# Kernel optimization log

Hardware: AMD Instinct MI355X
Metric: run time of the kernel (lower is better)

## Reference

```python
import jax, jax.numpy as jnp
import numpy as np

G = 8  # order of C8 rotation group

def expand_circulant(w):
    # w: [out_fields, in_fields, G] free params of a C8 regular->regular 1x1 conv.
    # Full weight: W[of*G+go, if*G+gi] = w[of, if, (go-gi) mod G]
    g = jnp.arange(G)
    idx = (g[:, None] - g[None, :]) % G            # [go, gi]
    Wf = w[:, :, idx]                              # [of, if, go, gi]
    Wf = jnp.transpose(Wf, (0, 2, 1, 3))           # [of, go, if, gi]
    return Wf.reshape(w.shape[0] * G, w.shape[1] * G)

def eq_proj(x2, w, b):
    # x2: [B, in_fields*G]; equivariant 1x1 conv = GEMM with circulant-expanded weight
    Wf = expand_circulant(w)                       # [out_fields*G, in_fields*G]
    bf = jnp.repeat(b, G)                          # per-field bias, shared across group dim
    return x2 @ Wf.T + bf

def setup_inputs() -> dict:
    key = jax.random.key(0)
    ks = jax.random.split(key, 12)
    B, d_model, n_head, d_k, d_v = 8192, 128, 8, 64, 64
    C = d_model * G                                # 1024
    s_in = 0.02
    inp = {
        'q': jax.random.normal(ks[0], (B, C, 1, 1), jnp.float32),
        'k': jax.random.normal(ks[1], (B, C, 1, 1), jnp.float32),
        'v': jax.random.normal(ks[2], (B, C, 1, 1), jnp.float32),
        'w_q': jax.random.normal(ks[3], (n_head * d_k, d_model, G), jnp.float32) * s_in,
        'b_q': jnp.zeros((n_head * d_k,), jnp.float32),
        'w_k': jax.random.normal(ks[4], (n_head * d_k, d_model, G), jnp.float32) * s_in,
        'b_k': jnp.zeros((n_head * d_k,), jnp.float32),
        'w_v': jax.random.normal(ks[5], (n_head * d_v, d_model, G), jnp.float32) * s_in,
        'b_v': jnp.zeros((n_head * d_v,), jnp.float32),
        'w_fc': jax.random.normal(ks[6], (d_model, n_head * d_v, G), jnp.float32) * s_in,
        'b_fc': jnp.zeros((d_model,), jnp.float32),
    }
    return inp

def reference(q, k, v, w_q, b_q, w_k, b_k, w_v, b_v, w_fc, b_fc):
    B, C = q.shape[0], q.shape[1]
    n_head, d_k = 8, 64
    d_v = 64
    temp = jnp.asarray(d_k ** 0.5, q.dtype)
    residual = q                                   # [B, C, 1, 1]
    q2 = q.reshape(B, C)
    k2 = k.reshape(B, C)
    v2 = v.reshape(B, C)
    # equivariant 1x1 conv projections -> [B, n_head*d_k*G]
    qp = eq_proj(q2, w_q, b_q).reshape(B, G, n_head, d_k).transpose(0, 2, 1, 3)  # [B,H,G,dk]
    kp = eq_proj(k2, w_k, b_k).reshape(B, G, n_head, d_k).transpose(0, 2, 1, 3)
    vp = eq_proj(v2, w_v, b_v).reshape(B, G, n_head, d_v).transpose(0, 2, 1, 3)
    # scaled dot-product attention over the G=8 group/orientation positions
    attn = jax.nn.softmax(jnp.einsum('bhqd,bhkd->bhqk', qp / temp, kp), axis=-1)  # [B,H,G,G]
    out = jnp.einsum('bhqk,bhkd->bhqd', attn, vp)  # [B,H,G,dv]
    # transpose(1,2) then flatten, exactly as torch .view(sz_b, -1, 1, 1)
    out = out.transpose(0, 2, 1, 3).reshape(B, G * n_head * d_v)
    out = eq_proj(out, w_fc, b_fc)                 # [B, d_model*G]
    out = out.reshape(B, C, 1, 1) + residual
    return out, attn
```

## Files before the change

kernel.cpp:

```cpp
#include <hip/hip_runtime.h>
#include <hip/hip_bf16.h>

typedef unsigned short u16;
typedef unsigned int u32;
typedef __bf16 bf16x8_t __attribute__((ext_vector_type(8)));
typedef float f32x4_t __attribute__((ext_vector_type(4)));

#define BK 64

__device__ __forceinline__ float b2f(u16 v) {
  return __uint_as_float(((u32)v) << 16);
}
__device__ __forceinline__ u16 f2b(float f) {
  __hip_bfloat16 h = __float2bfloat16(f);
  return *reinterpret_cast<u16*>(&h);
}
__device__ __forceinline__ float blo(u32 u) { return __uint_as_float(u << 16); }
__device__ __forceinline__ float bhi(u32 u) { return __uint_as_float(u & 0xffff0000u); }

__device__ __forceinline__ void async_lds16(const u16* g, u16* l) {
  __builtin_amdgcn_global_load_lds(
      (__attribute__((address_space(1))) void*)g,
      (__attribute__((address_space(3))) void*)l, 16, 0, 0);
}

__device__ __forceinline__ void expand8(const float* __restrict__ w,
                                        u16* __restrict__ dst, int I,
                                        int kshift, int gid) {
  const int n = gid >> kshift;
  const int kc = (gid & ((1 << kshift) - 1)) * 8;
  const int K = 8 << kshift;
  const float* wp = w + (size_t)((n >> 3) * I + (kc >> 3)) * 8;
  float4 w0 = *(const float4*)wp;
  float4 w1 = *(const float4*)(wp + 4);
  float w8[8] = {w0.x, w0.y, w0.z, w0.w, w1.x, w1.y, w1.z, w1.w};
  u16 t[8];
  const int r = (n - kc) & 7;
#pragma unroll
  for (int j = 0; j < 8; ++j) t[j] = f2b(w8[(r - j) & 7]);
  *(uint4*)(dst + (size_t)n * K + kc) = *(const uint4*)t;
}

__device__ __forceinline__ void cvt8(const float* __restrict__ src,
                                     u16* __restrict__ dst, int gid) {
  const float* p = src + (size_t)gid * 8;
  float4 a = *(const float4*)p;
  float4 b = *(const float4*)(p + 4);
  u16 t[8] = {f2b(a.x), f2b(a.y), f2b(a.z), f2b(a.w),
              f2b(b.x), f2b(b.y), f2b(b.z), f2b(b.w)};
  *(uint4*)(dst + (size_t)gid * 8) = *(const uint4*)t;
}

__global__ __launch_bounds__(256) void expand_all(
    const float* __restrict__ w_q, const float* __restrict__ w_k,
    const float* __restrict__ w_v, const float* __restrict__ w_fc,
    const float* __restrict__ q, const float* __restrict__ k,
    const float* __restrict__ v, u16* __restrict__ Wq, u16* __restrict__ Wk,
    u16* __restrict__ Wv, u16* __restrict__ Wfc, u16* __restrict__ qb,
    u16* __restrict__ kb, u16* __restrict__ vb, int cblocks) {
  const int e = blockIdx.x;
  if (e < 8192) {
    const int plane = e >> 11;
    const int gid = (e & 2047) * 256 + threadIdx.x;
    if (plane == 0) expand8(w_q, Wq, 128, 7, gid);
    else if (plane == 1) expand8(w_k, Wk, 128, 7, gid);
    else if (plane == 2) expand8(w_v, Wv, 128, 7, gid);
    else expand8(w_fc, Wfc, 512, 9, gid);
  } else {
    const int ce = e - 8192;
    const int plane = ce / cblocks;
    const int gid = (ce - plane * cblocks) * 256 + threadIdx.x;
    if (plane == 0) cvt8(q, qb, gid);
    else if (plane == 1) cvt8(k, kb, gid);
    else cvt8(v, vb, gid);
  }
}

__global__ __launch_bounds__(512, 2) void gemm_qkv256(
    const u16* __restrict__ X0, const u16* __restrict__ X1,
    const u16* __restrict__ X2, const u16* __restrict__ W0,
    const u16* __restrict__ W1, const u16* __restrict__ W2,
    const float* __restrict__ b0, const float* __restrict__ b1,
    const float* __restrict__ b2, u16* __restrict__ Y0, u16* __restrict__ Y1,
    u16* __restrict__ Y2, int M, int N, int K) {
  __shared__ __align__(16) u16 lds[4 * 16384];
  const int z = blockIdx.y;
  const u16* X = (z == 0) ? X0 : (z == 1) ? X1 : X2;
  const u16* W = (z == 0) ? W0 : (z == 1) ? W1 : W2;
  const float* bias = (z == 0) ? b0 : (z == 1) ? b1 : b2;
  u16* Y = (z == 0) ? Y0 : (z == 1) ? Y1 : Y2;

  const int tid = threadIdx.x;
  const int bid = blockIdx.x;
  const int grid_m = M >> 8, grid_n = N >> 8;
  const int nb = grid_m * grid_n;
  int pid = (bid & 7) * (nb >> 3) + (bid >> 3);
  const int nig = 8 * grid_n;
  const int group_id = pid / nig;
  const int first_m = group_id * 8;
  const int gsz = min(8, grid_m - first_m);
  const int mt = first_m + (pid % gsz);
  const int ntile = (pid % nig) / gsz;
  const int m0 = mt << 8, n0 = ntile << 8;

  const int lane = tid & 63, wave = tid >> 6;
  const int wm = (wave >> 2) * 128;
  const int wn = (wave & 3) * 64;
  const int l16 = lane & 15, quad = lane >> 4;
  const int kbl = quad ^ ((l16 >> 1) & 3);

  const int srow = tid >> 2;
  const int skbg = (tid & 3) ^ ((tid >> 3) & 3);
  const u16* pA = X + (size_t)(m0 + srow) * K + skbg * 8;
  const u16* pB = W + (size_t)(n0 + srow) * K + skbg * 8;
  const size_t rskip = (size_t)128 * K;

  const int aoff = (wm + l16) * 32 + kbl * 8;
  const int boff = 8192 + (wn + l16) * 32 + kbl * 8;

  f32x4_t acc[8][4] = {};
  const int nt = K >> 5;

  auto stage = [&](int t) {
    u16* l = lds + (t & 3) * 16384;
    const u16* a = pA + t * 32;
    const u16* b = pB + t * 32;
    async_lds16(a, l + tid * 8);
    async_lds16(a + rskip, l + tid * 8 + 4096);
    async_lds16(b, l + 8192 + tid * 8);
    async_lds16(b + rskip, l + 8192 + tid * 8 + 4096);
  };

  bf16x8_t A0[4], A1[4], Bc[4], Bn[4];

  stage(0);
  __builtin_amdgcn_sched_barrier(0);
  stage(1);
  __builtin_amdgcn_sched_barrier(0);
  stage(2);
  asm volatile("s_waitcnt vmcnt(4)" ::: "memory");
  __builtin_amdgcn_s_barrier();
  __builtin_amdgcn_sched_barrier(0);

  {
    const u16* la = lds + aoff;
    const u16* lb = lds + boff;
#pragma unroll
    for (int mi = 0; mi < 4; ++mi) A0[mi] = *(const bf16x8_t*)(la + mi * 512);
#pragma unroll
    for (int ni = 0; ni < 4; ++ni) Bc[ni] = *(const bf16x8_t*)(lb + ni * 512);
  }

  auto body = [&](int t, bf16x8_t (&BCUR)[4], bf16x8_t (&BNXT)[4]) {
    if (t + 3 < nt) stage(t + 3);
    const u16* lc = lds + (t & 3) * 16384;
    const u16* ln = lds + ((t + 1) & 3) * 16384;
#pragma unroll
    for (int mi = 0; mi < 4; ++mi)
      A1[mi] = *(const bf16x8_t*)(lc + aoff + (mi + 4) * 512);
    if (t + 1 < nt) {
#pragma unroll
      for (int ni = 0; ni < 4; ++ni)
        BNXT[ni] = *(const bf16x8_t*)(ln + boff + ni * 512);
    }
    __builtin_amdgcn_s_setprio(1);
#pragma unroll
    for (int mi = 0; mi < 4; ++mi)
#pragma unroll
      for (int ni = 0; ni < 4; ++ni)
        acc[mi][ni] = __builtin_amdgcn_mfma_f32_16x16x32_bf16(
            A0[mi], BCUR[ni], acc[mi][ni], 0, 0, 0);
    __builtin_amdgcn_s_setprio(0);
    if (t + 1 < nt) {
#pragma unroll
      for (int mi = 0; mi < 4; ++mi)
        A0[mi] = *(const bf16x8_t*)(ln + aoff + mi * 512);
    }
    __builtin_amdgcn_s_setprio(1);
#pragma unroll
    for (int mi = 0; mi < 4; ++mi)
#pragma unroll
      for (int ni = 0; ni < 4; ++ni)
        acc[mi + 4][ni] = __builtin_amdgcn_mfma_f32_16x16x32_bf16(
            A1[mi], BCUR[ni], acc[mi + 4][ni], 0, 0, 0);
    __builtin_amdgcn_s_setprio(0);
    if (t + 1 < nt) {
      asm volatile("s_waitcnt lgkmcnt(0)" ::: "memory");
      __builtin_amdgcn_sched_barrier(0);
      if (t + 3 < nt) asm volatile("s_waitcnt vmcnt(4)" ::: "memory");
      else            asm volatile("s_waitcnt vmcnt(0)" ::: "memory");
      __builtin_amdgcn_s_barrier();
      __builtin_amdgcn_sched_barrier(0);
    }
  };

  for (int t = 0; t < nt; t += 2) {
    body(t, Bc, Bn);
    body(t + 1, Bn, Bc);
  }

#pragma unroll
  for (int ni = 0; ni < 4; ++ni) {
    const int col = n0 + wn + ni * 16 + l16;
    const float bv = bias[col >> 3];
#pragma unroll
    for (int mi = 0; mi < 8; ++mi) {
#pragma unroll
      for (int r = 0; r < 4; ++r) {
        const int rw = m0 + wm + mi * 16 + quad * 4 + r;
        Y[(size_t)rw * N + col] = f2b(acc[mi][ni][r] + bv);
      }
    }
  }
}

template <int TN, bool HAS_RES, bool OUT_F32>
__device__ __forceinline__ void gemm_core(
    const u16* __restrict__ Xb, const u16* __restrict__ W,
    const float* __restrict__ bias, const float* __restrict__ res,
    void* __restrict__ Yv, int M, int N, int K, int bid) {
  __shared__ __align__(16) u16 As[128 * BK];
  __shared__ __align__(16) u16 Bs[TN * BK];
  const int tid = threadIdx.x;

  const int grid_m = M >> 7, grid_n = N / TN;
  const int nb = grid_m * grid_n;
  int pid = (bid & 7) * (nb >> 3) + (bid >> 3);
  const int nig = 8 * grid_n;
  const int group_id = pid / nig;
  const int first_m = group_id * 8;
  const int gsz = min(8, grid_m - first_m);
  const int mt = first_m + (pid % gsz);
  const int nt = (pid % nig) / gsz;
  const int m0 = mt << 7, n0 = nt * TN;

  const int lane = tid & 63;
  const int wave = tid >> 6;
  const int wm = (wave >> 1) * 64;
  const int wn = (wave & 1) * (TN / 2);
  const int l16 = lane & 15;
  const int quad = lane >> 4;
  constexpr int NJ = TN >> 5;

  f32x4_t acc[4][NJ] = {};

  const int row0 = tid >> 3;
  const int kgl = ((tid & 7) ^ (row0 & 7)) * 8;

  for (int k0 = 0; k0 < K; k0 += BK) {
#pragma unroll
    for (int it = 0; it < TN / 32; ++it)
      async_lds16(W + (size_t)(n0 + row0 + it * 32) * K + (k0 + kgl),
                  &Bs[(tid + it * 256) * 8]);
#pragma unroll
    for (int it = 0; it < 4; ++it)
      async_lds16(Xb + (size_t)(m0 + row0 + it * 32) * K + (k0 + kgl),
                  &As[(tid + it * 256) * 8]);
    __syncthreads();
#pragma unroll
    for (int half = 0; half < 2; ++half) {
      bf16x8_t af[4], bfr[NJ];
#pragma unroll
      for (int i = 0; i < 4; ++i)
        af[i] = *(const bf16x8_t*)&As[(wm + i * 16 + l16) * BK +
                                      (((quad + half * 4) ^ (l16 & 7)) * 8)];
#pragma unroll
      for (int j = 0; j < NJ; ++j)
        bfr[j] = *(const bf16x8_t*)&Bs[(wn + j * 16 + l16) * BK +
                                       (((quad + half * 4) ^ (l16 & 7)) * 8)];
#pragma unroll
      for (int i = 0; i < 4; ++i)
#pragma unroll
        for (int j = 0; j < NJ; ++j)
          acc[i][j] =
              __builtin_amdgcn_mfma_f32_16x16x32_bf16(af[i], bfr[j], acc[i][j], 0, 0, 0);
    }
    __syncthreads();
  }

#pragma unroll
  for (int j = 0; j < NJ; ++j) {
    const int col = n0 + wn + j * 16 + l16;
    const float bv = bias[col >> 3];
#pragma unroll
    for (int i = 0; i < 4; ++i) {
#pragma unroll
      for (int r = 0; r < 4; ++r) {
        const int rw = m0 + wm + i * 16 + quad * 4 + r;
        float vv = acc[i][j][r] + bv;
        if (HAS_RES) vv += res[(size_t)rw * N + col];
        if (OUT_F32)
          ((float*)Yv)[(size_t)rw * N + col] = vv;
        else
          ((u16*)Yv)[(size_t)rw * N + col] = f2b(vv);
      }
    }
  }
}

__global__ __launch_bounds__(256) void gemm_fc(
    const u16* __restrict__ X, const u16* __restrict__ W,
    const float* __restrict__ bias, const float* __restrict__ res,
    float* __restrict__ Y, int M, int N, int K) {
  gemm_core<64, true, true>(X, W, bias, res, Y, M, N, K, blockIdx.x);
}

__global__ __launch_bounds__(256) void attn_kernel(
    const u16* __restrict__ qp, const u16* __restrict__ kp,
    const u16* __restrict__ vp, float* __restrict__ probs,
    u16* __restrict__ o, int iters) {
  __shared__ __align__(16) u16 Qs[4][8 * 72];
  __shared__ __align__(16) u16 Ks[4][8 * 72];
  __shared__ __align__(16) float Ps[4][64];
  const int tid = threadIdx.x;
  const int wave = tid >> 6;
  const int lane = tid & 63;
  const int r = lane >> 3, c = lane & 7;
  const int ls = r * 72 + c * 8;
  const int qg = r;
  const int kg = c;

  auto pairof = [&](int it) { return (it * gridDim.x + blockIdx.x) * 4 + wave; };
  auto gaddr = [&](int it) {
    const int pr = pairof(it);
    return (size_t)(pr >> 3) * 4096 + (size_t)r * 512 + (pr & 7) * 64 + c * 8;
  };

  uint4 qr = *(const uint4*)(qp + gaddr(0));
  uint4 kr = *(const uint4*)(kp + gaddr(0));

  for (int it = 0; it < iters; ++it) {
    *(uint4*)&Qs[wave][ls] = qr;
    *(uint4*)&Ks[wave][ls] = kr;
    const int pair = pairof(it);
    const int b = pair >> 3;
    const int h = pair & 7;
    float vcf[8];
#pragma unroll
    for (int k2 = 0; k2 < 8; ++k2)
      vcf[k2] = b2f(vp[(size_t)b * 4096 + (size_t)k2 * 512 + h * 64 + lane]);
    if (it + 1 < iters) {
      qr = *(const uint4*)(qp + gaddr(it + 1));
      kr = *(const uint4*)(kp + gaddr(it + 1));
    }
    float s = 0.f;
#pragma unroll
    for (int d8 = 0; d8 < 8; ++d8) {
      uint4 qa = *(const uint4*)&Qs[wave][qg * 72 + d8 * 8];
      uint4 ka = *(const uint4*)&Ks[wave][kg * 72 + d8 * 8];
      s += blo(qa.x) * blo(ka.x) + bhi(qa.x) * bhi(ka.x);
      s += blo(qa.y) * blo(ka.y) + bhi(qa.y) * bhi(ka.y);
      s += blo(qa.z) * blo(ka.z) + bhi(qa.z) * bhi(ka.z);
      s += blo(qa.w) * blo(ka.w) + bhi(qa.w) * bhi(ka.w);
    }
    s *= 0.125f;
    float mx = s;
    mx = fmaxf(mx, __shfl_xor(mx, 1));
    mx = fmaxf(mx, __shfl_xor(mx, 2));
    mx = fmaxf(mx, __shfl_xor(mx, 4));
    float e = __expf(s - mx);
    float sum = e;
    sum += __shfl_xor(sum, 1);
    sum += __shfl_xor(sum, 2);
    sum += __shfl_xor(sum, 4);
    const float p = e / sum;
    probs[(size_t)pair * 64 + lane] = p;
    Ps[wave][lane] = p;
#pragma unroll
    for (int q2 = 0; q2 < 8; ++q2) {
      float4 p0 = *(const float4*)&Ps[wave][q2 * 8];
      float4 p1 = *(const float4*)&Ps[wave][q2 * 8 + 4];
      float acc = p0.x * vcf[0] + p0.y * vcf[1] + p0.z * vcf[2] + p0.w * vcf[3] +
                  p1.x * vcf[4] + p1.y * vcf[5] + p1.z * vcf[6] + p1.w * vcf[7];
      o[(size_t)b * 4096 + q2 * 512 + h * 64 + lane] = f2b(acc);
    }
  }
}

extern "C" void kernel_launch(void* const* d_in, const int* in_sizes, int n_in,
                              void* d_out, int out_size, void* d_ws, size_t ws_size,
                              hipStream_t stream) {
  const float* q = (const float*)d_in[0];
  const float* k = (const float*)d_in[1];
  const float* v = (const float*)d_in[2];
  const float* w_q = (const float*)d_in[3];
  const float* b_q = (const float*)d_in[4];
  const float* w_k = (const float*)d_in[5];
  const float* b_k = (const float*)d_in[6];
  const float* w_v = (const float*)d_in[7];
  const float* b_v = (const float*)d_in[8];
  const float* w_fc = (const float*)d_in[9];
  const float* b_fc = (const float*)d_in[10];

  const int B = in_sizes[0] / 1024;
  float* out = (float*)d_out;
  float* probs = out + (size_t)B * 1024;

  u16* Wq = (u16*)d_ws;
  u16* Wk = Wq + (size_t)4096 * 1024;
  u16* Wv = Wk + (size_t)4096 * 1024;
  u16* Wfc = Wv + (size_t)4096 * 1024;
  u16* qb = Wfc + (size_t)4096 * 1024;
  u16* kb = qb + (size_t)B * 1024;
  u16* vb = kb + (size_t)B * 1024;
  u16* scratch = vb + (size_t)B * 1024;
  const size_t fixed_bytes =
      ((size_t)4 * 4096 * 1024 + (size_t)3 * B * 1024) * sizeof(u16);

  const size_t per_row = (size_t)(4 * 4096) * sizeof(u16);
  int chunkB = 256;
  for (int c = B; c >= 256; c >>= 1) {
    if (fixed_bytes + (size_t)c * per_row <= ws_size) { chunkB = c; break; }
  }

  u16* qp = scratch;
  u16* kp = qp + (size_t)chunkB * 4096;
  u16* vp = kp + (size_t)chunkB * 4096;
  u16* ao = vp + (size_t)chunkB * 4096;

  const int cblocks = B / 2;
  expand_all<<<8192 + 3 * cblocks, 256, 0, stream>>>(
      w_q, w_k, w_v, w_fc, q, k, v, Wq, Wk, Wv, Wfc, qb, kb, vb, cblocks);

  for (int cs = 0; cs < B; cs += chunkB) {
    const int nb_p = (chunkB / 256) * (4096 / 256);
    gemm_qkv256<<<dim3(nb_p, 3), 512, 0, stream>>>(
        qb + (size_t)cs * 1024, kb + (size_t)cs * 1024, vb + (size_t)cs * 1024,
        Wq, Wk, Wv, b_q, b_k, b_v, qp, kp, vp, chunkB, 4096, 1024);
    const int ablocks = (chunkB >= 1024) ? 2048 : chunkB * 2;
    const int aiters = (chunkB * 8) / (ablocks * 4);
    attn_kernel<<<ablocks, 256, 0, stream>>>(qp, kp, vp,
                                             probs + (size_t)cs * 512, ao, aiters);
    const int nb_fc = (chunkB / 128) * (1024 / 64);
    gemm_fc<<<nb_fc, 256, 0, stream>>>(ao, Wfc, b_fc, q + (size_t)cs * 1024,
                                       out + (size_t)cs * 1024, chunkB, 1024,
                                       4096);
  }
}
```

Measured before the change: 617.3 us.

## Reuse 4-stage pipelined MFMA GEMM template for the output projection

Turns the async 4-buffer pipelined QKV GEMM into a template over tile sizes and uses it for the fc projection too, with 256x128 tiles and 512 threads. This replaces the old fc GEMM, which loaded and computed each K-step in sequence between syncthreads barriers with no overlap. The fc GEMM has K=4096, so latency hiding should help it. The trade-offs are fewer blocks for the fc launch and higher register and LDS use per block.

```diff
diff --git a/kernel.cpp b/kernel.cpp
--- a/kernel.cpp
+++ b/kernel.cpp
@@ -5,8 +5,6 @@
 typedef unsigned int u32;
 typedef __bf16 bf16x8_t __attribute__((ext_vector_type(8)));
 typedef float f32x4_t __attribute__((ext_vector_type(4)));
-
-#define BK 64
 
 __device__ __forceinline__ float b2f(u16 v) {
   return __uint_as_float(((u32)v) << 16);
@@ -76,23 +74,20 @@
   }
 }
 
-__global__ __launch_bounds__(512, 2) void gemm_qkv256(
-    const u16* __restrict__ X0, const u16* __restrict__ X1,
-    const u16* __restrict__ X2, const u16* __restrict__ W0,
-    const u16* __restrict__ W1, const u16* __restrict__ W2,
-    const float* __restrict__ b0, const float* __restrict__ b1,
-    const float* __restrict__ b2, u16* __restrict__ Y0, u16* __restrict__ Y1,
-    u16* __restrict__ Y2, int M, int N, int K) {
-  __shared__ __align__(16) u16 lds[4 * 16384];
-  const int z = blockIdx.y;
-  const u16* X = (z == 0) ? X0 : (z == 1) ? X1 : X2;
-  const u16* W = (z == 0) ? W0 : (z == 1) ? W1 : W2;
-  const float* bias = (z == 0) ? b0 : (z == 1) ? b1 : b2;
-  u16* Y = (z == 0) ? Y0 : (z == 1) ? Y1 : Y2;
+template <int TM, int TN, bool HAS_RES, bool OUT_F32>
+__device__ __forceinline__ void gemm_pipe(
+    const u16* __restrict__ X, const u16* __restrict__ W,
+    const float* __restrict__ bias, const float* __restrict__ res,
+    void* __restrict__ Yv, int M, int N, int K, int bid) {
+  constexpr int LDS_A = TM * 32;
+  constexpr int BUF = (TM + TN) * 32;
+  constexpr int APASS = TM / 128, BPASS = TN / 128;
+  constexpr int LPT = APASS + BPASS;
+  constexpr int NJ = TN / 64;
+  __shared__ __align__(16) u16 lds[4 * BUF];
 
   const int tid = threadIdx.x;
-  const int bid = blockIdx.x;
-  const int grid_m = M >> 8, grid_n = N >> 8;
+  const int grid_m = M / TM, grid_n = N / TN;
   const int nb = grid_m * grid_n;
   int pid = (bid & 7) * (nb >> 3) + (bid >> 3);
   const int nig = 8 * grid_n;
@@ -101,11 +96,11 @@
   const int gsz = min(8, grid_m - first_m);
   const int mt = first_m + (pid % gsz);
   const int ntile = (pid % nig) / gsz;
-  const int m0 = mt << 8, n0 = ntile << 8;
+  const int m0 = mt * TM, n0 = ntile * TN;
 
   const int lane = tid & 63, wave = tid >> 6;
-  const int wm = (wave >> 2) * 128;
-  const int wn = (wave & 3) * 64;
+  const int wm = (wave >> 2) * (TM / 2);
+  const int wn = (wave & 3) * (TN / 4);
   const int l16 = lane & 15, quad = lane >> 4;
   const int kbl = quad ^ ((l16 >> 1) & 3);
 
@@ -116,29 +111,41 @@
   const size_t rskip = (size_t)128 * K;
 
   const int aoff = (wm + l16) * 32 + kbl * 8;
-  const int boff = 8192 + (wn + l16) * 32 + kbl * 8;
-
-  f32x4_t acc[8][4] = {};
+  const int boff = LDS_A + (wn + l16) * 32 + kbl * 8;
+
+  f32x4_t acc[8][NJ] = {};
   const int nt = K >> 5;
 
   auto stage = [&](int t) {
-    u16* l = lds + (t & 3) * 16384;
+    u16* l = lds + (t & 3) * BUF;
     const u16* a = pA + t * 32;
     const u16* b = pB + t * 32;
-    async_lds16(a, l + tid * 8);
-    async_lds16(a + rskip, l + tid * 8 + 4096);
-    async_lds16(b, l + 8192 + tid * 8);
-    async_lds16(b + rskip, l + 8192 + tid * 8 + 4096);
+#pragma unroll
+    for (int p = 0; p < APASS; ++p)
+      async_lds16(a + p * rskip, l + tid * 8 + p * 4096);
+#pragma unroll
+    for (int p = 0; p < BPASS; ++p)
+      async_lds16(b + p * rskip, l + LDS_A + tid * 8 + p * 4096);
   };
 
-  bf16x8_t A0[4], A1[4], Bc[4], Bn[4];
+#define WAIT_VM_LPT()                                              \
+  do {                                                             \
+    if constexpr (LPT == 4)                                        \
+      asm volatile("s_waitcnt vmcnt(4)" ::: "memory");             \
+    else if constexpr (LPT == 3)                                   \
+      asm volatile("s_waitcnt vmcnt(3)" ::: "memory");             \
+    else                                                           \
+      asm volatile("s_waitcnt vmcnt(2)" ::: "memory");             \
+  } while (0)
+
+  bf16x8_t A0[4], A1[4], Bc[NJ], Bn[NJ];
 
   stage(0);
   __builtin_amdgcn_sched_barrier(0);
   stage(1);
   __builtin_amdgcn_sched_barrier(0);
   stage(2);
-  asm volatile("s_waitcnt vmcnt(4)" ::: "memory");
+  WAIT_VM_LPT();
   __builtin_amdgcn_s_barrier();
   __builtin_amdgcn_sched_barrier(0);
 
@@ -148,26 +155,26 @@
 #pragma unroll
     for (int mi = 0; mi < 4; ++mi) A0[mi] = *(const bf16x8_t*)(la + mi * 512);
 #pragma unroll
-    for (int ni = 0; ni < 4; ++ni) Bc[ni] = *(const bf16x8_t*)(lb + ni * 512);
-  }
-
-  auto body = [&](int t, bf16x8_t (&BCUR)[4], bf16x8_t (&BNXT)[4]) {
+    for (int ni = 0; ni < NJ; ++ni) Bc[ni] = *(const bf16x8_t*)(lb + ni * 512);
+  }
+
+  auto body = [&](int t, bf16x8_t (&BCUR)[NJ], bf16x8_t (&BNXT)[NJ]) {
     if (t + 3 < nt) stage(t + 3);
-    const u16* lc = lds + (t & 3) * 16384;
-    const u16* ln = lds + ((t + 1) & 3) * 16384;
+    const u16* lc = lds + (t & 3) * BUF;
+    const u16* ln = lds + ((t + 1) & 3) * BUF;
 #pragma unroll
     for (int mi = 0; mi < 4; ++mi)
       A1[mi] = *(const bf16x8_t*)(lc + aoff + (mi + 4) * 512);
     if (t + 1 < nt) {
 #pragma unroll
-      for (int ni = 0; ni < 4; ++ni)
+      for (int ni = 0; ni < NJ; ++ni)
         BNXT[ni] = *(const bf16x8_t*)(ln + boff + ni * 512);
     }
     __builtin_amdgcn_s_setprio(1);
 #pragma unroll
     for (int mi = 0; mi < 4; ++mi)
 #pragma unroll
-      for (int ni = 0; ni < 4; ++ni)
+      for (int ni = 0; ni < NJ; ++ni)
         acc[mi][ni] = __builtin_amdgcn_mfma_f32_16x16x32_bf16(
             A0[mi], BCUR[ni], acc[mi][ni], 0, 0, 0);
     __builtin_amdgcn_s_setprio(0);
@@ -180,14 +187,14 @@
 #pragma unroll
     for (int mi = 0; mi < 4; ++mi)
 #pragma unroll
-      for (int ni = 0; ni < 4; ++ni)
+      for (int ni = 0; ni < NJ; ++ni)
         acc[mi + 4][ni] = __builtin_amdgcn_mfma_f32_16x16x32_bf16(
             A1[mi], BCUR[ni], acc[mi + 4][ni], 0, 0, 0);
     __builtin_amdgcn_s_setprio(0);
     if (t + 1 < nt) {
       asm volatile("s_waitcnt lgkmcnt(0)" ::: "memory");
       __builtin_amdgcn_sched_barrier(0);
-      if (t + 3 < nt) asm volatile("s_waitcnt vmcnt(4)" ::: "memory");
+      if (t + 3 < nt) WAIT_VM_LPT();
       else            asm volatile("s_waitcnt vmcnt(0)" ::: "memory");
       __builtin_amdgcn_s_barrier();
       __builtin_amdgcn_sched_barrier(0);
@@ -198,9 +205,10 @@
     body(t, Bc, Bn);
     body(t + 1, Bn, Bc);
   }
-
-#pragma unroll
-  for (int ni = 0; ni < 4; ++ni) {
+#undef WAIT_VM_LPT
+
+#pragma unroll
+  for (int ni = 0; ni < NJ; ++ni) {
     const int col = n0 + wn + ni * 16 + l16;
     const float bv = bias[col >> 3];
 #pragma unroll
@@ -208,86 +216,7 @@
 #pragma unroll
       for (int r = 0; r < 4; ++r) {
         const int rw = m0 + wm + mi * 16 + quad * 4 + r;
-        Y[(size_t)rw * N + col] = f2b(acc[mi][ni][r] + bv);
-      }
-    }
-  }
-}
-
-template <int TN, bool HAS_RES, bool OUT_F32>
-__device__ __forceinline__ void gemm_core(
-    const u16* __restrict__ Xb, const u16* __restrict__ W,
-    const float* __restrict__ bias, const float* __restrict__ res,
-    void* __restrict__ Yv, int M, int N, int K, int bid) {
-  __shared__ __align__(16) u16 As[128 * BK];
-  __shared__ __align__(16) u16 Bs[TN * BK];
-  const int tid = threadIdx.x;
-
-  const int grid_m = M >> 7, grid_n = N / TN;
-  const int nb = grid_m * grid_n;
-  int pid = (bid & 7) * (nb >> 3) + (bid >> 3);
-  const int nig = 8 * grid_n;
-  const int group_id = pid / nig;
-  const int first_m = group_id * 8;
-  const int gsz = min(8, grid_m - first_m);
-  const int mt = first_m + (pid % gsz);
-  const int nt = (pid % nig) / gsz;
-  const int m0 = mt << 7, n0 = nt * TN;
-
-  const int lane = tid & 63;
-  const int wave = tid >> 6;
-  const int wm = (wave >> 1) * 64;
-  const int wn = (wave & 1) * (TN / 2);
-  const int l16 = lane & 15;
-  const int quad = lane >> 4;
-  constexpr int NJ = TN >> 5;
-
-  f32x4_t acc[4][NJ] = {};
-
-  const int row0 = tid >> 3;
-  const int kgl = ((tid & 7) ^ (row0 & 7)) * 8;
-
-  for (int k0 = 0; k0 < K; k0 += BK) {
-#pragma unroll
-    for (int it = 0; it < TN / 32; ++it)
-      async_lds16(W + (size_t)(n0 + row0 + it * 32) * K + (k0 + kgl),
-                  &Bs[(tid + it * 256) * 8]);
-#pragma unroll
-    for (int it = 0; it < 4; ++it)
-      async_lds16(Xb + (size_t)(m0 + row0 + it * 32) * K + (k0 + kgl),
-                  &As[(tid + it * 256) * 8]);
-    __syncthreads();
-#pragma unroll
-    for (int half = 0; half < 2; ++half) {
-      bf16x8_t af[4], bfr[NJ];
-#pragma unroll
-      for (int i = 0; i < 4; ++i)
-        af[i] = *(const bf16x8_t*)&As[(wm + i * 16 + l16) * BK +
-                                      (((quad + half * 4) ^ (l16 & 7)) * 8)];
-#pragma unroll
-      for (int j = 0; j < NJ; ++j)
-        bfr[j] = *(const bf16x8_t*)&Bs[(wn + j * 16 + l16) * BK +
-                                       (((quad + half * 4) ^ (l16 & 7)) * 8)];
-#pragma unroll
-      for (int i = 0; i < 4; ++i)
-#pragma unroll
-        for (int j = 0; j < NJ; ++j)
-          acc[i][j] =
-              __builtin_amdgcn_mfma_f32_16x16x32_bf16(af[i], bfr[j], acc[i][j], 0, 0, 0);
-    }
-    __syncthreads();
-  }
-
-#pragma unroll
-  for (int j = 0; j < NJ; ++j) {
-    const int col = n0 + wn + j * 16 + l16;
-    const float bv = bias[col >> 3];
-#pragma unroll
-    for (int i = 0; i < 4; ++i) {
-#pragma unroll
-      for (int r = 0; r < 4; ++r) {
-        const int rw = m0 + wm + i * 16 + quad * 4 + r;
-        float vv = acc[i][j][r] + bv;
+        float vv = acc[mi][ni][r] + bv;
         if (HAS_RES) vv += res[(size_t)rw * N + col];
         if (OUT_F32)
           ((float*)Yv)[(size_t)rw * N + col] = vv;
@@ -298,11 +227,26 @@
   }
 }
 
-__global__ __launch_bounds__(256) void gemm_fc(
+__global__ __launch_bounds__(512, 2) void gemm_qkv256(
+    const u16* __restrict__ X0, const u16* __restrict__ X1,
+    const u16* __restrict__ X2, const u16* __restrict__ W0,
+    const u16* __restrict__ W1, const u16* __restrict__ W2,
+    const float* __restrict__ b0, const float* __restrict__ b1,
+    const float* __restrict__ b2, u16* __restrict__ Y0, u16* __restrict__ Y1,
+    u16* __restrict__ Y2, int M, int N, int K) {
+  const int z = blockIdx.y;
+  const u16* X = (z == 0) ? X0 : (z == 1) ? X1 : X2;
+  const u16* W = (z == 0) ? W0 : (z == 1) ? W1 : W2;
+  const float* bb = (z == 0) ? b0 : (z == 1) ? b1 : b2;
+  u16* Y = (z == 0) ? Y0 : (z == 1) ? Y1 : Y2;
+  gemm_pipe<256, 256, false, false>(X, W, bb, nullptr, Y, M, N, K, blockIdx.x);
+}
+
+__global__ __launch_bounds__(512, 2) void gemm_fc(
     const u16* __restrict__ X, const u16* __restrict__ W,
     const float* __restrict__ bias, const float* __restrict__ res,
     float* __restrict__ Y, int M, int N, int K) {
-  gemm_core<64, true, true>(X, W, bias, res, Y, M, N, K, blockIdx.x);
+  gemm_pipe<256, 128, true, true>(X, W, bias, res, Y, M, N, K, blockIdx.x);
 }
 
 __global__ __launch_bounds__(256) void attn_kernel(
@@ -431,8 +375,8 @@
     const int aiters = (chunkB * 8) / (ablocks * 4);
     attn_kernel<<<ablocks, 256, 0, stream>>>(qp, kp, vp,
                                              probs + (size_t)cs * 512, ao, aiters);
-    const int nb_fc = (chunkB / 128) * (1024 / 64);
-    gemm_fc<<<nb_fc, 256, 0, stream>>>(ao, Wfc, b_fc, q + (size_t)cs * 1024,
+    const int nb_fc = (chunkB / 256) * (1024 / 128);
+    gemm_fc<<<nb_fc, 512, 0, stream>>>(ao, Wfc, b_fc, q + (size_t)cs * 1024,
                                        out + (size_t)cs * 1024, chunkB, 1024,
                                        4096);
   }
```

New measurement: 643.7 us. +4.3%, slower.
